# Kernel tuning notes

Hardware: AMD Instinct MI355X
Metric: run time of the kernel (lower is better)

Reference implementation:

```python
import jax, jax.numpy as jnp
import numpy as np

N = 100000      # nodes in batch / feature table
S = 25          # sampled neighbors per node (nsamples)
F_IN = 128      # in_features
F_OUT = 128     # out_features


def setup_inputs() -> dict:
    key = jax.random.key(0)
    k1, k2, k3, k4 = jax.random.split(key, 4)
    x = jax.random.normal(k1, (N, F_IN), dtype=jnp.float32)
    neighbor_idx = jax.random.randint(k2, (N, S), 0, N, dtype=jnp.int64)
    stdv = 1.0 / np.sqrt(F_OUT)
    W = jax.random.uniform(k3, (F_IN, F_OUT), dtype=jnp.float32, minval=-stdv, maxval=stdv)
    b = jax.random.uniform(k4, (F_OUT,), dtype=jnp.float32, minval=-stdv, maxval=stdv)
    return {"x": x, "neighbor_idx": neighbor_idx, "W": W, "b": b}


def reference(x, neighbor_idx, W, b):
    # GraphSage-style mean aggregator: gather sampled neighbor features
    # [N, S, F_IN], average together with the self feature, then project.
    neigh = jnp.take(x, neighbor_idx, axis=0)          # [N, S, F_IN] (irregular gather)
    agg = (x + neigh.sum(axis=1)) / jnp.float32(S + 1)  # mean over {self} U neighbors
    return agg @ W + b                                  # [N, F_OUT]
```

## Files before the change

kernel.cpp:

```cpp
#include <hip/hip_runtime.h>

#define F 128
#define S 25
#define CH 4
#define CW 32

typedef __attribute__((ext_vector_type(8))) short bf16x8;
typedef __attribute__((ext_vector_type(4))) float f32x4;

__device__ __forceinline__ ushort f2bf(float f) {
    uint u = __float_as_uint(f);
    return (ushort)((u + 0x7FFFu + ((u >> 16) & 1u)) >> 16);
}
__device__ __forceinline__ float bf_lo(uint v) { return __uint_as_float(v << 16); }
__device__ __forceinline__ float bf_hi(uint v) { return __uint_as_float(v & 0xFFFF0000u); }

__device__ __forceinline__ bool idx_is_i64(const int* __restrict__ p) {
    return (p[1] | p[3] | p[5] | p[7]) == 0;
}
__device__ __forceinline__ int load_idx(const int* __restrict__ p, size_t i, bool is64) {
    return is64 ? p[2 * i] : p[i];
}

__global__ __launch_bounds__(256) void compact_idx(
    const int* __restrict__ src, int* __restrict__ dst, int M)
{
    const bool is64 = idx_is_i64(src);
    int e = blockIdx.x * 256 + threadIdx.x;
    if (e < M) dst[e] = load_idx(src, (size_t)e, is64);
}

__global__ __launch_bounds__(256) void pack_W(
    const float* __restrict__ W, ushort* __restrict__ WFg)
{
    const int id = blockIdx.x * 256 + threadIdx.x;
    if (id >= 4 * 8 * 64) return;
    const int l  = id & 63;
    const int nt = (id >> 6) & 7;
    const int kt = id >> 9;
    const int k0 = kt * 32 + (l >> 4) * 8;
    const int nn = nt * 16 + (l & 15);
    bf16x8 fr;
    #pragma unroll
    for (int b = 0; b < 8; ++b)
        fr[b] = (short)f2bf(W[(size_t)(k0 + b) * F + nn]);
    *(bf16x8*)(WFg + (size_t)id * 8) = fr;
}

template <int CHUNKED>
__global__ __launch_bounds__(256) void gemm_xw_bf16(
    const float* __restrict__ x, const ushort* __restrict__ WFg,
    ushort* __restrict__ y, int N)
{
    __shared__ ushort WF[4][8][64][8];

    const int tid  = threadIdx.x;
    const int lane = tid & 63;
    const int wid  = tid >> 6;

    {
        const bf16x8* src = (const bf16x8*)WFg;
        bf16x8* dst = (bf16x8*)&WF[0][0][0][0];
        #pragma unroll
        for (int i = 0; i < 8; ++i)
            dst[tid + 256 * i] = src[tid + 256 * i];
    }
    __syncthreads();

    const int n0 = blockIdx.x * 64 + wid * 16;
    const int arow = n0 + (lane & 15);
    const int arow_c = arow < N ? arow : N - 1;
    const float* xrow = x + (size_t)arow_c * F + (lane >> 4) * 8;

    f32x4 acc[8];
    #pragma unroll
    for (int nt = 0; nt < 8; ++nt) acc[nt] = (f32x4){0.f, 0.f, 0.f, 0.f};

    #pragma unroll
    for (int kt = 0; kt < 4; ++kt) {
        float4 a0 = *(const float4*)(xrow + kt * 32);
        float4 a1 = *(const float4*)(xrow + kt * 32 + 4);
        bf16x8 af;
        af[0] = (short)f2bf(a0.x); af[1] = (short)f2bf(a0.y);
        af[2] = (short)f2bf(a0.z); af[3] = (short)f2bf(a0.w);
        af[4] = (short)f2bf(a1.x); af[5] = (short)f2bf(a1.y);
        af[6] = (short)f2bf(a1.z); af[7] = (short)f2bf(a1.w);
        #pragma unroll
        for (int nt = 0; nt < 8; ++nt) {
            bf16x8 bf = *(const bf16x8*)&WF[kt][nt][lane][0];
            acc[nt] = __builtin_amdgcn_mfma_f32_16x16x32_bf16(af, bf, acc[nt], 0, 0, 0);
        }
    }

    const int drow0 = n0 + (lane >> 4) * 4;
    const int dcol  = lane & 15;
    #pragma unroll
    for (int nt = 0; nt < 8; ++nt) {
        #pragma unroll
        for (int r = 0; r < 4; ++r) {
            const int row = drow0 + r;
            if (row < N) {
                if (CHUNKED) {
                    y[((size_t)(nt >> 1) * N + row) * CW + (nt & 1) * 16 + dcol] = f2bf(acc[nt][r]);
                } else {
                    y[(size_t)row * F + nt * 16 + dcol] = f2bf(acc[nt][r]);
                }
            }
        }
    }
}

__global__ __launch_bounds__(256) void gather_chunked(
    const ushort* __restrict__ y, const int* __restrict__ idx32,
    const float* __restrict__ bias, float* __restrict__ out, int N)
{
    __shared__ int IDX[64 * S];

    const int tid   = threadIdx.x;
    const int chunk = blockIdx.x & (CH - 1);
    const int tile  = blockIdx.x >> 2;
    const int nbase = tile * 64;
    const long total = (long)N * S;

    for (int e = tid; e < 64 * S; e += 256) {
        long p = (long)nbase * S + e;
        IDX[e] = (p < total) ? __builtin_nontemporal_load(&idx32[p]) : 0;
    }
    __syncthreads();

    const int lane = tid & 63, wave = tid >> 6;
    const int g = lane >> 3, j = lane & 7;
    const float inv = 1.0f / (float)(S + 1);
    const char* ycb = (const char*)(y + (size_t)chunk * N * CW);
    const uint joff = (uint)(j << 3);
    const f32x4 bb = *(const f32x4*)(bias + chunk * CW + 4 * j);

    #pragma unroll
    for (int oct = 0; oct < 2; ++oct) {
        const int nl = wave * 16 + oct * 8 + g;
        const int n  = nbase + nl;
        const int nc = n < N ? n : 0;

        uint2 v[26];
        v[25] = *(const uint2*)(ycb + (((uint)nc) << 6) + joff);
        #pragma unroll
        for (int s = 0; s < S; ++s) {
            const uint id = (uint)IDX[nl * S + s];
            v[s] = *(const uint2*)(ycb + (id << 6) + joff);
        }

        float a0 = 0.f, a1 = 0.f, a2 = 0.f, a3 = 0.f;
        #pragma unroll
        for (int s = 0; s < 26; ++s) {
            a0 += bf_lo(v[s].x); a1 += bf_hi(v[s].x);
            a2 += bf_lo(v[s].y); a3 += bf_hi(v[s].y);
        }

        if (n < N) {
            f32x4 o = {a0 * inv + bb.x, a1 * inv + bb.y,
                       a2 * inv + bb.z, a3 * inv + bb.w};
            __builtin_nontemporal_store(
                o, (f32x4*)(out + (size_t)n * F + chunk * CW + 4 * j));
        }
    }
}

__global__ __launch_bounds__(256) void gather_agg_bf16(
    const ushort* __restrict__ y, const int* __restrict__ nbr,
    const float* __restrict__ bias, float* __restrict__ out, int N)
{
    const int lane = threadIdx.x & 63;
    const int wid  = threadIdx.x >> 6;
    const bool is64 = idx_is_i64(nbr);
    const float2 bb = ((const float2*)bias)[lane];
    const float inv = 1.0f / (float)(S + 1);
    const int nw = gridDim.x * 4;
    const uint* yw = (const uint*)y;

    for (int n = blockIdx.x * 4 + wid; n < N; n += nw) {
        const int nu = __builtin_amdgcn_readfirstlane(n);
        int ids[S];
        #pragma unroll
        for (int s = 0; s < S; ++s)
            ids[s] = load_idx(nbr, (size_t)nu * S + s, is64);
        uint vs[S];
        #pragma unroll
        for (int s = 0; s < S; ++s)
            vs[s] = yw[(size_t)ids[s] * 64 + lane];
        const uint v0 = yw[(size_t)nu * 64 + lane];
        float ax = bf_lo(v0), ay = bf_hi(v0);
        #pragma unroll
        for (int s = 0; s < S; ++s) { ax += bf_lo(vs[s]); ay += bf_hi(vs[s]); }
        float2 o;
        o.x = ax * inv + bb.x;
        o.y = ay * inv + bb.y;
        ((float2*)(out + (size_t)nu * F))[lane] = o;
    }
}

__global__ __launch_bounds__(256) void fused_fallback_kernel(
    const float* __restrict__ x, const int* __restrict__ nbr,
    const float* __restrict__ W, const float* __restrict__ bias,
    float* __restrict__ out, int N)
{
    __shared__ float aggs[4][F];
    const int lane = threadIdx.x & 63;
    const int wid  = threadIdx.x >> 6;
    const bool is64 = idx_is_i64(nbr);
    const float inv = 1.0f / (float)(S + 1);
    const int stride = gridDim.x * 4;

    for (int base = blockIdx.x * 4; base < N; base += stride) {
        int n = base + wid;
        bool act = n < N;
        float2 acc = make_float2(0.f, 0.f);
        if (act) {
            acc = ((const float2*)(x + (size_t)n * F))[lane];
            for (int s = 0; s < S; ++s) {
                int id = load_idx(nbr, (size_t)n * S + s, is64);
                float2 v = ((const float2*)(x + (size_t)id * F))[lane];
                acc.x += v.x; acc.y += v.y;
            }
        }
        aggs[wid][2 * lane]     = acc.x * inv;
        aggs[wid][2 * lane + 1] = acc.y * inv;
        __syncthreads();
        if (act) {
            float o0 = bias[lane], o1 = bias[lane + 64];
            for (int k = 0; k < F; ++k) {
                float a = aggs[wid][k];
                o0 += a * W[k * F + lane];
                o1 += a * W[k * F + lane + 64];
            }
            out[(size_t)n * F + lane]      = o0;
            out[(size_t)n * F + lane + 64] = o1;
        }
        __syncthreads();
    }
}

extern "C" void kernel_launch(void* const* d_in, const int* in_sizes, int n_in,
                              void* d_out, int out_size, void* d_ws, size_t ws_size,
                              hipStream_t stream) {
    const float* x    = (const float*)d_in[0];
    const int*   nbr  = (const int*)d_in[1];
    const float* W    = (const float*)d_in[2];
    const float* bias = (const float*)d_in[3];
    float* out = (float*)d_out;
    const int N = in_sizes[0] / F;
    const int M = N * S;

    const size_t y_bytes   = (size_t)N * F * sizeof(ushort);
    const size_t idx_bytes = (size_t)M * sizeof(int);
    const size_t wf_bytes  = (size_t)4 * 8 * 64 * 8 * sizeof(ushort);

    if (ws_size >= y_bytes + idx_bytes + wf_bytes) {
        ushort* y    = (ushort*)d_ws;
        int*   idx32 = (int*)((char*)d_ws + y_bytes);
        ushort* WFg  = (ushort*)((char*)d_ws + y_bytes + idx_bytes);
        compact_idx<<<(M + 255) / 256, 256, 0, stream>>>(nbr, idx32, M);
        pack_W<<<8, 256, 0, stream>>>(W, WFg);
        gemm_xw_bf16<1><<<(N + 63) / 64, 256, 0, stream>>>(x, WFg, y, N);
        const int tiles = (N + 63) / 64;
        gather_chunked<<<tiles * CH, 256, 0, stream>>>(y, idx32, bias, out, N);
    } else if (ws_size >= y_bytes + wf_bytes) {
        ushort* y   = (ushort*)d_ws;
        ushort* WFg = (ushort*)((char*)d_ws + y_bytes);
        pack_W<<<8, 256, 0, stream>>>(W, WFg);
        gemm_xw_bf16<0><<<(N + 63) / 64, 256, 0, stream>>>(x, WFg, y, N);
        gather_agg_bf16<<<2048, 256, 0, stream>>>(y, nbr, bias, out, N);
    } else {
        fused_fallback_kernel<<<2048, 256, 0, stream>>>(x, nbr, W, bias, out, N);
    }
}
```

Before: 115.1 us.

## Drop index compaction, widen gather chunks, stage GEMM output through LDS

Result: faster. 102.3 us (-11.2%).

```diff
diff --git a/kernel.cpp b/kernel.cpp
--- a/kernel.cpp
+++ b/kernel.cpp
@@ -2,8 +2,8 @@
 
 #define F 128
 #define S 25
-#define CH 4
-#define CW 32
+#define CH 2
+#define CW 64
 
 typedef __attribute__((ext_vector_type(8))) short bf16x8;
 typedef __attribute__((ext_vector_type(4))) float f32x4;
@@ -20,14 +20,6 @@
 }
 __device__ __forceinline__ int load_idx(const int* __restrict__ p, size_t i, bool is64) {
     return is64 ? p[2 * i] : p[i];
-}
-
-__global__ __launch_bounds__(256) void compact_idx(
-    const int* __restrict__ src, int* __restrict__ dst, int M)
-{
-    const bool is64 = idx_is_i64(src);
-    int e = blockIdx.x * 256 + threadIdx.x;
-    if (e < M) dst[e] = load_idx(src, (size_t)e, is64);
 }
 
 __global__ __launch_bounds__(256) void pack_W(
@@ -52,7 +44,8 @@
     const float* __restrict__ x, const ushort* __restrict__ WFg,
     ushort* __restrict__ y, int N)
 {
-    __shared__ ushort WF[4][8][64][8];
+    __shared__ __align__(16) ushort WF[4][8][64][8];
+    __shared__ __align__(16) ushort Ytile[64][136];
 
     const int tid  = threadIdx.x;
     const int lane = tid & 63;
@@ -92,61 +85,80 @@
         }
     }
 
-    const int drow0 = n0 + (lane >> 4) * 4;
-    const int dcol  = lane & 15;
+    const int lr0  = wid * 16 + (lane >> 4) * 4;
+    const int dcol = lane & 15;
     #pragma unroll
     for (int nt = 0; nt < 8; ++nt) {
         #pragma unroll
-        for (int r = 0; r < 4; ++r) {
-            const int row = drow0 + r;
-            if (row < N) {
-                if (CHUNKED) {
-                    y[((size_t)(nt >> 1) * N + row) * CW + (nt & 1) * 16 + dcol] = f2bf(acc[nt][r]);
-                } else {
-                    y[(size_t)row * F + nt * 16 + dcol] = f2bf(acc[nt][r]);
-                }
+        for (int r = 0; r < 4; ++r)
+            Ytile[lr0 + r][nt * 16 + dcol] = f2bf(acc[nt][r]);
+    }
+    __syncthreads();
+
+    const int n0b = blockIdx.x * 64;
+    #pragma unroll
+    for (int i = 0; i < 4; ++i) {
+        const int e   = i * 256 + tid;
+        const int row = e >> 4, seg = e & 15;
+        const int n   = n0b + row;
+        if (n < N) {
+            bf16x8 val = *(const bf16x8*)&Ytile[row][seg * 8];
+            if (CHUNKED) {
+                const int c = seg >> 3;
+                const int ccol = (seg & 7) * 8;
+                *(bf16x8*)&y[((size_t)c * N + n) * CW + ccol] = val;
+            } else {
+                *(bf16x8*)&y[(size_t)n * F + seg * 8] = val;
             }
         }
     }
 }
 
 __global__ __launch_bounds__(256) void gather_chunked(
-    const ushort* __restrict__ y, const int* __restrict__ idx32,
+    const ushort* __restrict__ y, const int* __restrict__ nbr,
     const float* __restrict__ bias, float* __restrict__ out, int N)
 {
     __shared__ int IDX[64 * S];
 
     const int tid   = threadIdx.x;
     const int chunk = blockIdx.x & (CH - 1);
-    const int tile  = blockIdx.x >> 2;
+    const int tile  = blockIdx.x >> 1;
     const int nbase = tile * 64;
     const long total = (long)N * S;
-
-    for (int e = tid; e < 64 * S; e += 256) {
-        long p = (long)nbase * S + e;
-        IDX[e] = (p < total) ? __builtin_nontemporal_load(&idx32[p]) : 0;
+    const bool is64 = idx_is_i64(nbr);
+
+    if (is64) {
+        for (int e = tid; e < 64 * S; e += 256) {
+            long p = (long)nbase * S + e;
+            IDX[e] = (p < total) ? __builtin_nontemporal_load(&nbr[2 * p]) : 0;
+        }
+    } else {
+        for (int e = tid; e < 64 * S; e += 256) {
+            long p = (long)nbase * S + e;
+            IDX[e] = (p < total) ? __builtin_nontemporal_load(&nbr[p]) : 0;
+        }
     }
     __syncthreads();
 
     const int lane = tid & 63, wave = tid >> 6;
-    const int g = lane >> 3, j = lane & 7;
+    const int g = lane >> 4, j = lane & 15;
     const float inv = 1.0f / (float)(S + 1);
     const char* ycb = (const char*)(y + (size_t)chunk * N * CW);
     const uint joff = (uint)(j << 3);
     const f32x4 bb = *(const f32x4*)(bias + chunk * CW + 4 * j);
 
     #pragma unroll
-    for (int oct = 0; oct < 2; ++oct) {
-        const int nl = wave * 16 + oct * 8 + g;
+    for (int q = 0; q < 4; ++q) {
+        const int nl = wave * 16 + q * 4 + g;
         const int n  = nbase + nl;
         const int nc = n < N ? n : 0;
 
         uint2 v[26];
-        v[25] = *(const uint2*)(ycb + (((uint)nc) << 6) + joff);
+        v[25] = *(const uint2*)(ycb + (((uint)nc) << 7) + joff);
         #pragma unroll
         for (int s = 0; s < S; ++s) {
             const uint id = (uint)IDX[nl * S + s];
-            v[s] = *(const uint2*)(ycb + (id << 6) + joff);
+            v[s] = *(const uint2*)(ycb + (id << 7) + joff);
         }
 
         float a0 = 0.f, a1 = 0.f, a2 = 0.f, a3 = 0.f;
@@ -162,39 +174,6 @@
             __builtin_nontemporal_store(
                 o, (f32x4*)(out + (size_t)n * F + chunk * CW + 4 * j));
         }
-    }
-}
-
-__global__ __launch_bounds__(256) void gather_agg_bf16(
-    const ushort* __restrict__ y, const int* __restrict__ nbr,
-    const float* __restrict__ bias, float* __restrict__ out, int N)
-{
-    const int lane = threadIdx.x & 63;
-    const int wid  = threadIdx.x >> 6;
-    const bool is64 = idx_is_i64(nbr);
-    const float2 bb = ((const float2*)bias)[lane];
-    const float inv = 1.0f / (float)(S + 1);
-    const int nw = gridDim.x * 4;
-    const uint* yw = (const uint*)y;
-
-    for (int n = blockIdx.x * 4 + wid; n < N; n += nw) {
-        const int nu = __builtin_amdgcn_readfirstlane(n);
-        int ids[S];
-        #pragma unroll
-        for (int s = 0; s < S; ++s)
-            ids[s] = load_idx(nbr, (size_t)nu * S + s, is64);
-        uint vs[S];
-        #pragma unroll
-        for (int s = 0; s < S; ++s)
-            vs[s] = yw[(size_t)ids[s] * 64 + lane];
-        const uint v0 = yw[(size_t)nu * 64 + lane];
-        float ax = bf_lo(v0), ay = bf_hi(v0);
-        #pragma unroll
-        for (int s = 0; s < S; ++s) { ax += bf_lo(vs[s]); ay += bf_hi(vs[s]); }
-        float2 o;
-        o.x = ax * inv + bb.x;
-        o.y = ay * inv + bb.y;
-        ((float2*)(out + (size_t)nu * F))[lane] = o;
     }
 }
 
@@ -248,27 +227,17 @@
     const float* bias = (const float*)d_in[3];
     float* out = (float*)d_out;
     const int N = in_sizes[0] / F;
-    const int M = N * S;
-
-    const size_t y_bytes   = (size_t)N * F * sizeof(ushort);
-    const size_t idx_bytes = (size_t)M * sizeof(int);
-    const size_t wf_bytes  = (size_t)4 * 8 * 64 * 8 * sizeof(ushort);
-
-    if (ws_size >= y_bytes + idx_bytes + wf_bytes) {
-        ushort* y    = (ushort*)d_ws;
-        int*   idx32 = (int*)((char*)d_ws + y_bytes);
-        ushort* WFg  = (ushort*)((char*)d_ws + y_bytes + idx_bytes);
-        compact_idx<<<(M + 255) / 256, 256, 0, stream>>>(nbr, idx32, M);
-        pack_W<<<8, 256, 0, stream>>>(W, WFg);
-        gemm_xw_bf16<1><<<(N + 63) / 64, 256, 0, stream>>>(x, WFg, y, N);
-        const int tiles = (N + 63) / 64;
-        gather_chunked<<<tiles * CH, 256, 0, stream>>>(y, idx32, bias, out, N);
-    } else if (ws_size >= y_bytes + wf_bytes) {
+
+    const size_t y_bytes  = (size_t)N * F * sizeof(ushort);
+    const size_t wf_bytes = (size_t)4 * 8 * 64 * 8 * sizeof(ushort);
+
+    if (ws_size >= y_bytes + wf_bytes) {
         ushort* y   = (ushort*)d_ws;
         ushort* WFg = (ushort*)((char*)d_ws + y_bytes);
         pack_W<<<8, 256, 0, stream>>>(W, WFg);
-        gemm_xw_bf16<0><<<(N + 63) / 64, 256, 0, stream>>>(x, WFg, y, N);
-        gather_agg_bf16<<<2048, 256, 0, stream>>>(y, nbr, bias, out, N);
+        const int tiles = (N + 63) / 64;
+        gemm_xw_bf16<1><<<tiles, 256, 0, stream>>>(x, WFg, y, N);
+        gather_chunked<<<tiles * CH, 256, 0, stream>>>(y, nbr, bias, out, N);
     } else {
         fused_fallback_kernel<<<2048, 256, 0, stream>>>(x, nbr, W, bias, out, N);
     }
```
